# Kernel optimization log

Hardware: AMD Instinct MI355X
Metric: run time of the kernel (lower is better)

The kernel has to match this reference:

```python
import jax, jax.numpy as jnp
import numpy as np

B, S, D = 4, 8192, 768
H, HD = 12, 64
CS, NL = 512, 32


def setup_inputs() -> dict:
    key = jax.random.key(0)
    ks = jax.random.split(key, 9)
    sc = 0.02
    return {
        "x": jax.random.normal(ks[0], (B, S, D), jnp.float32),
        "q_w": jax.random.normal(ks[1], (D, D), jnp.float32) * sc,
        "q_b": jax.random.normal(ks[2], (D,), jnp.float32) * sc,
        "k_w": jax.random.normal(ks[3], (D, D), jnp.float32) * sc,
        "k_b": jax.random.normal(ks[4], (D,), jnp.float32) * sc,
        "v_w": jax.random.normal(ks[5], (D, D), jnp.float32) * sc,
        "v_b": jax.random.normal(ks[6], (D,), jnp.float32) * sc,
        "o_w": jax.random.normal(ks[7], (D, D), jnp.float32) * sc,
        "o_b": jax.random.normal(ks[8], (D,), jnp.float32) * sc,
    }


def reference(x, q_w, q_b, k_w, k_b, v_w, v_b, o_w, o_b):
    # x: (B, S, D); S divisible by CS and NL -> no padding / trimming needed.
    scale = HD ** -0.5
    n_chunks = S // CS
    seg = S // NL
    # Global landmarks: mean-pool NL evenly spaced segments. (B, NL, D)
    landmarks = x.reshape(B, NL, seg, D).mean(axis=2)
    # Q only over local tokens (torch Linear: x @ W^T + b)
    q = (x @ q_w.T + q_b).reshape(B, n_chunks, CS, H, HD)
    x_chunks = x.reshape(B, n_chunks, CS, D)
    # Prepend landmarks to every chunk's KV context: ctx = NL + CS
    lm = jnp.broadcast_to(landmarks[:, None], (B, n_chunks, NL, D))
    kv_ctx = jnp.concatenate([lm, x_chunks], axis=2)  # (B, n_chunks, ctx, D)
    ctx = NL + CS
    k = (kv_ctx @ k_w.T + k_b).reshape(B, n_chunks, ctx, H, HD)
    v = (kv_ctx @ v_w.T + v_b).reshape(B, n_chunks, ctx, H, HD)
    scores = jnp.einsum("bnqhd,bnkhd->bnhqk", q, k) * scale
    attn = jax.nn.softmax(scores, axis=-1)  # dropout=0 (eval)
    out = jnp.einsum("bnhqk,bnkhd->bnqhd", attn, v).reshape(B, S, D)
    return out @ o_w.T + o_b
```

## Files before the change

kernel.cpp:

```cpp
#include <hip/hip_runtime.h>


typedef unsigned short u16;
typedef __attribute__((ext_vector_type(8))) short short8;
typedef __attribute__((ext_vector_type(4))) float f32x4;

__device__ __forceinline__ u16 f2bf(float f) {
    unsigned u = __float_as_uint(f);
    u += 0x7fffu + ((u >> 16) & 1u);
    return (u16)(u >> 16);
}

#define MFMA_BF16(A, B, C) __builtin_amdgcn_mfma_f32_16x16x32_bf16((A), (B), (C), 0, 0, 0)

__device__ __forceinline__ void gload16(const u16* g, const short* l) {
    __builtin_amdgcn_global_load_lds(
        (__attribute__((address_space(1))) void*)g,
        (__attribute__((address_space(3))) void*)l, 16, 0, 0);
}

__global__ __launch_bounds__(256) void k_cvtx(const float* __restrict__ x,
                                              u16* __restrict__ xa,
                                              float* __restrict__ part) {
    const int g = blockIdx.x;
    const int t = threadIdx.x;
    const float* base = x + (size_t)g * 64 * 768;
    u16* ob = xa + (size_t)g * 64 * 768;
    float s0 = 0.f, s1 = 0.f, s2 = 0.f;
    for (int r = 0; r < 64; ++r) {
        const size_t off = (size_t)r * 768;
        const float v0 = base[off + t], v1 = base[off + t + 256], v2 = base[off + t + 512];
        s0 += v0; s1 += v1; s2 += v2;
        ob[off + t] = f2bf(v0); ob[off + t + 256] = f2bf(v1); ob[off + t + 512] = f2bf(v2);
    }
    float* p = part + (size_t)g * 768;
    p[t] = s0; p[t + 256] = s1; p[t + 512] = s2;
}

__global__ void k_lmred(const float* __restrict__ part, u16* __restrict__ xa_lm) {
    const int bl = blockIdx.x;
    const int t = threadIdx.x;
    const float* p = part + (size_t)bl * 4 * 768;
    const float inv = 1.f / 256.f;
    for (int c = t; c < 768; c += 256) {
        const float s = p[c] + p[768 + c] + p[1536 + c] + p[2304 + c];
        xa_lm[(size_t)bl * 768 + c] = f2bf(s * inv);
    }
}

__global__ void k_cvtw(const float* __restrict__ qw, const float* __restrict__ kw,
                       const float* __restrict__ vw, const float* __restrict__ ow,
                       const float* __restrict__ qb, const float* __restrict__ kb,
                       const float* __restrict__ vb,
                       u16* __restrict__ wcat, u16* __restrict__ owb,
                       float* __restrict__ bcat) {
    const int yy = blockIdx.y;
    const int i = blockIdx.x * 256 + threadIdx.x;
    if (yy == 4) {
        if (i < 768)       bcat[i] = qb[i];
        else if (i < 1536) bcat[i] = kb[i - 768];
        else if (i < 2304) bcat[i] = vb[i - 1536];
        return;
    }
    const float* src = (yy == 0) ? qw : (yy == 1) ? kw : (yy == 2) ? vw : ow;
    u16* dst = (yy == 3) ? owb : wcat + (size_t)yy * 589824;
    const float4 v = ((const float4*)src)[i];
    ushort4 o;
    o.x = f2bf(v.x); o.y = f2bf(v.y); o.z = f2bf(v.z); o.w = f2bf(v.w);
    ((ushort4*)dst)[i] = o;
}

template <int MODE>
__global__ __launch_bounds__(512, 1) void k_gemm(
    const u16* __restrict__ A, const u16* __restrict__ Bw, const float* __restrict__ bias,
    u16* __restrict__ qx, u16* __restrict__ ktok, u16* __restrict__ vt,
    u16* __restrict__ klm, u16* __restrict__ vlmt, float* __restrict__ outf)
{
    __shared__ short lA[2 * 16384];
    __shared__ short lB[2 * 16384];
    const int t = threadIdx.x;
    const int wid = t >> 6, lane = t & 63, lr = lane & 15, lg = lane >> 4;
    const int wm = wid >> 2, wn = wid & 3;

    const int gx = gridDim.x;
    const int nwg = gx * gridDim.y;
    const int orig = blockIdx.x + gx * blockIdx.y;
    const int qq = nwg >> 3, rr = nwg & 7, xcd = orig & 7, ii = orig >> 3;
    const int wg = (xcd < rr ? xcd * (qq + 1) : rr * (qq + 1) + (xcd - rr) * qq) + ii;
    const int m0 = (wg / gx) * 256, n0 = (wg % gx) * 256;

    const int MMAX = (MODE == 0) ? 32895 : 32767;
    const int u0 = t, u1 = 512 + t;
    const int r0 = u0 >> 3, c0 = ((u0 & 7) ^ (r0 & 7)) * 8;
    const int r1 = u1 >> 3, c1 = ((u1 & 7) ^ (r1 & 7)) * 8;
    const u16* pA[2][2]; const u16* pB[2][2];
#pragma unroll
    for (int h = 0; h < 2; ++h) {
        int ra0 = m0 + h * 128 + r0; if (ra0 > MMAX) ra0 = MMAX;
        int ra1 = m0 + h * 128 + r1; if (ra1 > MMAX) ra1 = MMAX;
        pA[h][0] = A + (size_t)ra0 * 768 + c0;
        pA[h][1] = A + (size_t)ra1 * 768 + c1;
        pB[h][0] = Bw + (size_t)(n0 + h * 128 + r0) * 768 + c0;
        pB[h][1] = Bw + (size_t)(n0 + h * 128 + r1) * 768 + c1;
    }
    const int sa0 = ((lg) ^ (lr & 7)) * 8;
    const int sa1 = ((4 + lg) ^ (lr & 7)) * 8;

#define STG_A(S, H, T) { gload16(pA[H][0] + (T) * 64, &lA[(S)*16384 + (H)*8192 + wid*512]);      \
                         gload16(pA[H][1] + (T) * 64, &lA[(S)*16384 + (H)*8192 + 4096 + wid*512]); }
#define STG_B(S, H, T) { gload16(pB[H][0] + (T) * 64, &lB[(S)*16384 + (H)*8192 + wid*512]);      \
                         gload16(pB[H][1] + (T) * 64, &lB[(S)*16384 + (H)*8192 + 4096 + wid*512]); }

    f32x4 acc[8][4] = {};
    short8 aq[4][2], bq[4][2];

    STG_A(0, 0, 0); STG_A(0, 1, 0); STG_B(0, 0, 0); STG_B(0, 1, 0);
    STG_A(1, 0, 1); STG_A(1, 1, 1);

#pragma unroll
    for (int T = 0; T < 12; ++T) {
        const int s = T & 1;
        const short* sa = &lA[s * 16384];
        const short* sbm = &lB[s * 16384];
        if (T + 1 < 12) STG_B(s ^ 1, 0, T + 1);
        if (T < 11) asm volatile("s_waitcnt vmcnt(6)" ::: "memory");
        else        asm volatile("s_waitcnt vmcnt(0)" ::: "memory");
        __builtin_amdgcn_s_barrier();
        __builtin_amdgcn_sched_barrier(0);
#pragma unroll
        for (int mf = 0; mf < 4; ++mf) {
            const int rb = (wm * 128 + mf * 16 + lr) * 64;
            aq[mf][0] = *(const short8*)&sa[rb + sa0];
            aq[mf][1] = *(const short8*)&sa[rb + sa1];
        }
#pragma unroll
        for (int nf = 0; nf < 4; ++nf) {
            const int rb = (wn * 64 + nf * 16 + lr) * 64;
            bq[nf][0] = *(const short8*)&sbm[rb + sa0];
            bq[nf][1] = *(const short8*)&sbm[rb + sa1];
        }
        __builtin_amdgcn_s_setprio(1);
#pragma unroll
        for (int mf = 0; mf < 4; ++mf)
#pragma unroll
            for (int nf = 0; nf < 2; ++nf)
#pragma unroll
                for (int kf = 0; kf < 2; ++kf)
                    acc[mf][nf] = MFMA_BF16(aq[mf][kf], bq[nf][kf], acc[mf][nf]);
        __builtin_amdgcn_s_setprio(0);
        if (T + 1 < 12) STG_B(s ^ 1, 1, T + 1);
        __builtin_amdgcn_s_barrier();
        __builtin_amdgcn_s_setprio(1);
#pragma unroll
        for (int mf = 0; mf < 4; ++mf)
#pragma unroll
            for (int nf = 2; nf < 4; ++nf)
#pragma unroll
                for (int kf = 0; kf < 2; ++kf)
                    acc[mf][nf] = MFMA_BF16(aq[mf][kf], bq[nf][kf], acc[mf][nf]);
        __builtin_amdgcn_s_setprio(0);
        __builtin_amdgcn_s_barrier();
#pragma unroll
        for (int mf = 0; mf < 4; ++mf) {
            const int rb = (wm * 128 + (mf + 4) * 16 + lr) * 64;
            aq[mf][0] = *(const short8*)&sa[rb + sa0];
            aq[mf][1] = *(const short8*)&sa[rb + sa1];
        }
        __builtin_amdgcn_s_setprio(1);
#pragma unroll
        for (int mf = 0; mf < 4; ++mf)
#pragma unroll
            for (int nf = 0; nf < 2; ++nf)
#pragma unroll
                for (int kf = 0; kf < 2; ++kf)
                    acc[mf + 4][nf] = MFMA_BF16(aq[mf][kf], bq[nf][kf], acc[mf + 4][nf]);
        __builtin_amdgcn_s_setprio(0);
        __builtin_amdgcn_s_barrier();
        if (T + 2 < 12) { STG_A(s, 0, T + 2); STG_A(s, 1, T + 2); }
        __builtin_amdgcn_s_setprio(1);
#pragma unroll
        for (int mf = 0; mf < 4; ++mf)
#pragma unroll
            for (int nf = 2; nf < 4; ++nf)
#pragma unroll
                for (int kf = 0; kf < 2; ++kf)
                    acc[mf + 4][nf] = MFMA_BF16(aq[mf][kf], bq[nf][kf], acc[mf + 4][nf]);
        __builtin_amdgcn_s_setprio(0);
    }
#undef STG_A
#undef STG_B

    if (MODE == 0) {
        const int region = n0 / 768;
        if (region == 2) {
#pragma unroll
            for (int nf = 0; nf < 4; ++nf) {
                const int gn = n0 + wn * 64 + nf * 16 + lr;
                const float bv = bias[gn];
                const int nn = gn - 1536;
                const int h = nn >> 6, d = nn & 63;
#pragma unroll
                for (int mf = 0; mf < 8; ++mf) {
                    const int gmb = m0 + wm * 128 + mf * 16 + lg * 4;
                    ushort4 w;
                    w.x = f2bf(acc[mf][nf][0] + bv);
                    w.y = f2bf(acc[mf][nf][1] + bv);
                    w.z = f2bf(acc[mf][nf][2] + bv);
                    w.w = f2bf(acc[mf][nf][3] + bv);
                    if (gmb < 32768) {
                        const int b = gmb >> 13, ss = gmb & 8191;
                        *(ushort4*)(vt + ((size_t)(b * 12 + h) * 64 + d) * 8192 + ss) = w;
                    } else if (gmb < 32896) {
                        const int ii2 = gmb - 32768;
                        const int bb = ii2 >> 5, lmr = ii2 & 31;
                        *(ushort4*)(vlmt + ((size_t)(bb * 12 + h) * 64 + d) * 32 + lmr) = w;
                    }
                }
            }
        } else {
            u16* dst = (region == 0) ? qx : ktok;
#pragma unroll
            for (int nf = 0; nf < 4; ++nf) {
                const int gn = n0 + wn * 64 + nf * 16 + lr;
                const int nn = gn - region * 768;
                const int h = nn >> 6, d = nn & 63;
                const float bv = bias[gn];
#pragma unroll
                for (int mf = 0; mf < 8; ++mf) {
                    const int gmb = m0 + wm * 128 + mf * 16 + lg * 4;
#pragma unroll
                    for (int r = 0; r < 4; ++r) {
                        const int gm = gmb + r;
                        const u16 val = f2bf(acc[mf][nf][r] + bv);
                        if (gm < 32768) {
                            const int b = gm >> 13, ss = gm & 8191;
                            dst[((size_t)(b * 12 + h) * 8192 + ss) * 64 + d] = val;
                        } else if (gm < 32896 && region == 1) {
                            const int ii2 = gm - 32768;
                            klm[((size_t)((ii2 >> 5) * 12 + h) * 32 + (ii2 & 31)) * 64 + d] = val;
                        }
                    }
                }
            }
        }
    } else {
#pragma unroll
        for (int nf = 0; nf < 4; ++nf) {
            const int gn = n0 + wn * 64 + nf * 16 + lr;
            const float bvv = bias[gn];
#pragma unroll
            for (int mf = 0; mf < 8; ++mf) {
                const int gmb = m0 + wm * 128 + mf * 16 + lg * 4;
#pragma unroll
                for (int r = 0; r < 4; ++r)
                    outf[(size_t)(gmb + r) * 768 + gn] = acc[mf][nf][r] + bvv;
            }
        }
    }
}

__global__ __launch_bounds__(256) void k_attn(
    const u16* __restrict__ q, const u16* __restrict__ ktok,
    const u16* __restrict__ klm, const u16* __restrict__ vt,
    const u16* __restrict__ vlmt, u16* __restrict__ ao)
{
    __shared__ short kls[2][32 * 72];
    __shared__ short vls[2][64 * 40];
    __shared__ short pls[4][64 * 40];
    const int t = threadIdx.x, wid = t >> 6, l = t & 63, lr = l & 15, lg = l >> 4;
    const int idx = blockIdx.x;
    const int qt = idx & 1;
    const int h  = (idx >> 1) % 12;
    const int cb = (idx >> 1) / 12;
    const int c  = cb & 15, b = cb >> 4;
    const int bh = b * 12 + h;
    const int sb = c * 512 + qt * 256 + wid * 64;

    short8 qf[4][2];
#pragma unroll
    for (int mf = 0; mf < 4; ++mf)
#pragma unroll
        for (int kf = 0; kf < 2; ++kf)
            qf[mf][kf] = *(const short8*)(q + ((size_t)bh * 8192 + sb + mf * 16 + lr) * 64
                                            + kf * 32 + lg * 8);

    f32x4 O[4][4] = {};
    float lsum[4][4] = {};

    short* pw = &pls[wid][0];
    const int kn = t >> 3, kko = (t & 7) * 8;
    const int kctx = (kn < 16) ? (kn * 2) : ((kn - 16) * 2 + 1);
    const int vd = t >> 2, vco = (t & 3) * 8;

    auto kaddr = [&](int ti) -> const u16* {
        if (ti == 0) return klm + ((size_t)bh * 32 + kctx) * 64 + kko;
        return ktok + ((size_t)bh * 8192 + c * 512 + (ti - 1) * 32 + kctx) * 64 + kko;
    };
    auto vaddr = [&](int ti) -> const u16* {
        if (ti == 0) return vlmt + ((size_t)bh * 64 + vd) * 32 + vco;
        return vt + ((size_t)bh * 64 + vd) * 8192 + c * 512 + (ti - 1) * 32 + vco;
    };

    {
        const uint4 rk0 = *(const uint4*)kaddr(0);
        const uint4 rv0 = *(const uint4*)vaddr(0);
        *(uint4*)&kls[0][kn * 72 + kko] = rk0;
        *(uint4*)&vls[0][vd * 40 + vco] = rv0;
    }
    __syncthreads();

    for (int ti = 0; ti < 17; ++ti) {
        const int cur = ti & 1, nxt = cur ^ 1;
        uint4 rk, rv;
        if (ti < 16) { rk = *(const uint4*)kaddr(ti + 1); rv = *(const uint4*)vaddr(ti + 1); }

        f32x4 sc[4][2] = {};
#pragma unroll
        for (int kf = 0; kf < 2; ++kf) {
            const short8 b0 = *(const short8*)&kls[cur][(lr)      * 72 + kf * 32 + lg * 8];
            const short8 b1 = *(const short8*)&kls[cur][(16 + lr) * 72 + kf * 32 + lg * 8];
#pragma unroll
            for (int mf = 0; mf < 4; ++mf) {
                sc[mf][0] = MFMA_BF16(qf[mf][kf], b0, sc[mf][0]);
                sc[mf][1] = MFMA_BF16(qf[mf][kf], b1, sc[mf][1]);
            }
        }

#pragma unroll
        for (int mf = 0; mf < 4; ++mf) {
#pragma unroll
            for (int r = 0; r < 4; ++r) {
                const float p0 = __expf(sc[mf][0][r] * 0.125f);
                const float p1 = __expf(sc[mf][1][r] * 0.125f);
                lsum[mf][r] += p0 + p1;
                unsigned pk;
                asm("v_cvt_pk_bf16_f32 %0, %1, %2" : "=v"(pk) : "v"(p0), "v"(p1));
                const int prow = mf * 16 + lg * 4 + r;
                ((unsigned*)pw)[prow * 20 + lr] = pk;
            }
        }

        short8 vb[4];
#pragma unroll
        for (int df = 0; df < 4; ++df)
            vb[df] = *(const short8*)&vls[cur][(df * 16 + lr) * 40 + lg * 8];
#pragma unroll
        for (int mf = 0; mf < 4; ++mf) {
            const short8 pa = *(const short8*)&pw[(mf * 16 + lr) * 40 + lg * 8];
#pragma unroll
            for (int df = 0; df < 4; ++df)
                O[mf][df] = MFMA_BF16(pa, vb[df], O[mf][df]);
        }

        if (ti < 16) {
            *(uint4*)&kls[nxt][kn * 72 + kko] = rk;
            *(uint4*)&vls[nxt][vd * 40 + vco] = rv;
        }
        __syncthreads();
    }

#pragma unroll
    for (int mf = 0; mf < 4; ++mf)
#pragma unroll
        for (int r = 0; r < 4; ++r) {
            float lv = lsum[mf][r];
            lv += __shfl_xor(lv, 1); lv += __shfl_xor(lv, 2);
            lv += __shfl_xor(lv, 4); lv += __shfl_xor(lv, 8);
            const float inv = 1.f / lv;
            const int srow = sb + mf * 16 + lg * 4 + r;
#pragma unroll
            for (int df = 0; df < 4; ++df)
                ao[((size_t)b * 8192 + srow) * 768 + h * 64 + df * 16 + lr] =
                    f2bf(O[mf][df][r] * inv);
        }
}

extern "C" void kernel_launch(void* const* d_in, const int* in_sizes, int n_in,
                              void* d_out, int out_size, void* d_ws, size_t ws_size,
                              hipStream_t stream)
{
    const float* x  = (const float*)d_in[0];
    const float* qw = (const float*)d_in[1];
    const float* qb = (const float*)d_in[2];
    const float* kw = (const float*)d_in[3];
    const float* kb = (const float*)d_in[4];
    const float* vw = (const float*)d_in[5];
    const float* vb = (const float*)d_in[6];
    const float* ow = (const float*)d_in[7];
    const float* ob = (const float*)d_in[8];
    float* out = (float*)d_out;

    u16* xa     = (u16*)d_ws;
    u16* wcat   = xa + (size_t)32896 * 768;
    u16* owb    = wcat + (size_t)2304 * 768;
    float* bcat = (float*)(owb + (size_t)768 * 768);
    u16* qx     = (u16*)(bcat + 2304);
    u16* ktok   = qx   + (size_t)32768 * 768;
    u16* vt     = ktok + (size_t)32768 * 768;
    u16* klm    = vt + (size_t)32768 * 768;
    u16* vlmt   = klm + 98304;
    float* part = (float*)(vlmt + 98304);
    u16* ao     = xa;

    k_cvtx<<<512, 256, 0, stream>>>(x, xa, part);
    k_lmred<<<128, 256, 0, stream>>>(part, xa + (size_t)32768 * 768);
    k_cvtw<<<dim3(576, 5), 256, 0, stream>>>(qw, kw, vw, ow, qb, kb, vb, wcat, owb, bcat);

    k_gemm<0><<<dim3(9, 129), 512, 0, stream>>>(xa, wcat, bcat,
                                                qx, ktok, vt, klm, vlmt, nullptr);
    k_attn<<<1536, 256, 0, stream>>>(qx, ktok, klm, vt, vlmt, ao);
    k_gemm<1><<<dim3(3, 128), 512, 0, stream>>>(ao, owb, ob,
                                                nullptr, nullptr, nullptr, nullptr, nullptr, out);
}
```

Before: 351.5 us.

## Shrink GEMM tiles to 128x128 with 256 threads and simpler double buffering

The projection GEMMs move from 256x256 tiles on 512-thread blocks to 128x128 tiles on 256-thread blocks with two blocks per CU. The interleaved split-phase pipeline with partial vmcnt waits is replaced by a plain double buffer that waits for all loads, then issues the next stage's loads before computing. The grids grow to match, and the row clamp for the 32896-row input is dropped because the tiles now divide it exactly. This trades per-tile data reuse and finely staged load/compute overlap for more blocks, better occupancy and less tail padding.

```diff
diff --git a/kernel.cpp b/kernel.cpp
--- a/kernel.cpp
+++ b/kernel.cpp
@@ -71,124 +71,79 @@
 }
 
 template <int MODE>
-__global__ __launch_bounds__(512, 1) void k_gemm(
+__global__ __launch_bounds__(256, 2) void k_gemm(
     const u16* __restrict__ A, const u16* __restrict__ Bw, const float* __restrict__ bias,
     u16* __restrict__ qx, u16* __restrict__ ktok, u16* __restrict__ vt,
     u16* __restrict__ klm, u16* __restrict__ vlmt, float* __restrict__ outf)
 {
-    __shared__ short lA[2 * 16384];
-    __shared__ short lB[2 * 16384];
+    __shared__ short lA[2][8192];
+    __shared__ short lB[2][8192];
     const int t = threadIdx.x;
     const int wid = t >> 6, lane = t & 63, lr = lane & 15, lg = lane >> 4;
-    const int wm = wid >> 2, wn = wid & 3;
+    const int wm = wid >> 1, wn = wid & 1;
 
     const int gx = gridDim.x;
     const int nwg = gx * gridDim.y;
     const int orig = blockIdx.x + gx * blockIdx.y;
     const int qq = nwg >> 3, rr = nwg & 7, xcd = orig & 7, ii = orig >> 3;
     const int wg = (xcd < rr ? xcd * (qq + 1) : rr * (qq + 1) + (xcd - rr) * qq) + ii;
-    const int m0 = (wg / gx) * 256, n0 = (wg % gx) * 256;
-
-    const int MMAX = (MODE == 0) ? 32895 : 32767;
-    const int u0 = t, u1 = 512 + t;
-    const int r0 = u0 >> 3, c0 = ((u0 & 7) ^ (r0 & 7)) * 8;
-    const int r1 = u1 >> 3, c1 = ((u1 & 7) ^ (r1 & 7)) * 8;
-    const u16* pA[2][2]; const u16* pB[2][2];
-#pragma unroll
-    for (int h = 0; h < 2; ++h) {
-        int ra0 = m0 + h * 128 + r0; if (ra0 > MMAX) ra0 = MMAX;
-        int ra1 = m0 + h * 128 + r1; if (ra1 > MMAX) ra1 = MMAX;
-        pA[h][0] = A + (size_t)ra0 * 768 + c0;
-        pA[h][1] = A + (size_t)ra1 * 768 + c1;
-        pB[h][0] = Bw + (size_t)(n0 + h * 128 + r0) * 768 + c0;
-        pB[h][1] = Bw + (size_t)(n0 + h * 128 + r1) * 768 + c1;
-    }
-    const int sa0 = ((lg) ^ (lr & 7)) * 8;
+    const int m0 = (wg / gx) * 128, n0 = (wg % gx) * 128;
+
+    const u16* pa[4]; const u16* pb[4];
+#pragma unroll
+    for (int j = 0; j < 4; ++j) {
+        const int u = j * 256 + t;
+        const int row = u >> 3, col = ((u & 7) ^ (row & 7)) * 8;
+        pa[j] = A  + (size_t)(m0 + row) * 768 + col;
+        pb[j] = Bw + (size_t)(n0 + row) * 768 + col;
+    }
+    const int sa0 = (lg ^ (lr & 7)) * 8;
     const int sa1 = ((4 + lg) ^ (lr & 7)) * 8;
 
-#define STG_A(S, H, T) { gload16(pA[H][0] + (T) * 64, &lA[(S)*16384 + (H)*8192 + wid*512]);      \
-                         gload16(pA[H][1] + (T) * 64, &lA[(S)*16384 + (H)*8192 + 4096 + wid*512]); }
-#define STG_B(S, H, T) { gload16(pB[H][0] + (T) * 64, &lB[(S)*16384 + (H)*8192 + wid*512]);      \
-                         gload16(pB[H][1] + (T) * 64, &lB[(S)*16384 + (H)*8192 + 4096 + wid*512]); }
-
-    f32x4 acc[8][4] = {};
-    short8 aq[4][2], bq[4][2];
-
-    STG_A(0, 0, 0); STG_A(0, 1, 0); STG_B(0, 0, 0); STG_B(0, 1, 0);
-    STG_A(1, 0, 1); STG_A(1, 1, 1);
+#define STG(S, T) {                                                       \
+    gload16(pa[0] + (T) * 64, &lA[S][0 * 2048 + wid * 512]);              \
+    gload16(pb[0] + (T) * 64, &lB[S][0 * 2048 + wid * 512]);              \
+    gload16(pa[1] + (T) * 64, &lA[S][1 * 2048 + wid * 512]);              \
+    gload16(pb[1] + (T) * 64, &lB[S][1 * 2048 + wid * 512]);              \
+    gload16(pa[2] + (T) * 64, &lA[S][2 * 2048 + wid * 512]);              \
+    gload16(pb[2] + (T) * 64, &lB[S][2 * 2048 + wid * 512]);              \
+    gload16(pa[3] + (T) * 64, &lA[S][3 * 2048 + wid * 512]);              \
+    gload16(pb[3] + (T) * 64, &lB[S][3 * 2048 + wid * 512]); }
+
+    f32x4 acc[4][4] = {};
+    STG(0, 0);
 
 #pragma unroll
     for (int T = 0; T < 12; ++T) {
         const int s = T & 1;
-        const short* sa = &lA[s * 16384];
-        const short* sbm = &lB[s * 16384];
-        if (T + 1 < 12) STG_B(s ^ 1, 0, T + 1);
-        if (T < 11) asm volatile("s_waitcnt vmcnt(6)" ::: "memory");
-        else        asm volatile("s_waitcnt vmcnt(0)" ::: "memory");
+        asm volatile("s_waitcnt vmcnt(0)" ::: "memory");
         __builtin_amdgcn_s_barrier();
         __builtin_amdgcn_sched_barrier(0);
+        if (T + 1 < 12) STG(s ^ 1, T + 1);
+        short8 aq[4][2], bq[4][2];
 #pragma unroll
         for (int mf = 0; mf < 4; ++mf) {
-            const int rb = (wm * 128 + mf * 16 + lr) * 64;
-            aq[mf][0] = *(const short8*)&sa[rb + sa0];
-            aq[mf][1] = *(const short8*)&sa[rb + sa1];
+            const int rb = (wm * 64 + mf * 16 + lr) * 64;
+            aq[mf][0] = *(const short8*)&lA[s][rb + sa0];
+            aq[mf][1] = *(const short8*)&lA[s][rb + sa1];
         }
 #pragma unroll
         for (int nf = 0; nf < 4; ++nf) {
             const int rb = (wn * 64 + nf * 16 + lr) * 64;
-            bq[nf][0] = *(const short8*)&sbm[rb + sa0];
-            bq[nf][1] = *(const short8*)&sbm[rb + sa1];
+            bq[nf][0] = *(const short8*)&lB[s][rb + sa0];
+            bq[nf][1] = *(const short8*)&lB[s][rb + sa1];
         }
         __builtin_amdgcn_s_setprio(1);
 #pragma unroll
         for (int mf = 0; mf < 4; ++mf)
 #pragma unroll
-            for (int nf = 0; nf < 2; ++nf)
+            for (int nf = 0; nf < 4; ++nf)
 #pragma unroll
                 for (int kf = 0; kf < 2; ++kf)
                     acc[mf][nf] = MFMA_BF16(aq[mf][kf], bq[nf][kf], acc[mf][nf]);
         __builtin_amdgcn_s_setprio(0);
-        if (T + 1 < 12) STG_B(s ^ 1, 1, T + 1);
-        __builtin_amdgcn_s_barrier();
-        __builtin_amdgcn_s_setprio(1);
-#pragma unroll
-        for (int mf = 0; mf < 4; ++mf)
-#pragma unroll
-            for (int nf = 2; nf < 4; ++nf)
-#pragma unroll
-                for (int kf = 0; kf < 2; ++kf)
-                    acc[mf][nf] = MFMA_BF16(aq[mf][kf], bq[nf][kf], acc[mf][nf]);
-        __builtin_amdgcn_s_setprio(0);
-        __builtin_amdgcn_s_barrier();
-#pragma unroll
-        for (int mf = 0; mf < 4; ++mf) {
-            const int rb = (wm * 128 + (mf + 4) * 16 + lr) * 64;
-            aq[mf][0] = *(const short8*)&sa[rb + sa0];
-            aq[mf][1] = *(const short8*)&sa[rb + sa1];
-        }
-        __builtin_amdgcn_s_setprio(1);
-#pragma unroll
-        for (int mf = 0; mf < 4; ++mf)
-#pragma unroll
-            for (int nf = 0; nf < 2; ++nf)
-#pragma unroll
-                for (int kf = 0; kf < 2; ++kf)
-                    acc[mf + 4][nf] = MFMA_BF16(aq[mf][kf], bq[nf][kf], acc[mf + 4][nf]);
-        __builtin_amdgcn_s_setprio(0);
-        __builtin_amdgcn_s_barrier();
-        if (T + 2 < 12) { STG_A(s, 0, T + 2); STG_A(s, 1, T + 2); }
-        __builtin_amdgcn_s_setprio(1);
-#pragma unroll
-        for (int mf = 0; mf < 4; ++mf)
-#pragma unroll
-            for (int nf = 2; nf < 4; ++nf)
-#pragma unroll
-                for (int kf = 0; kf < 2; ++kf)
-                    acc[mf + 4][nf] = MFMA_BF16(aq[mf][kf], bq[nf][kf], acc[mf + 4][nf]);
-        __builtin_amdgcn_s_setprio(0);
-    }
-#undef STG_A
-#undef STG_B
+    }
+#undef STG
 
     if (MODE == 0) {
         const int region = n0 / 768;
@@ -200,8 +155,8 @@
                 const int nn = gn - 1536;
                 const int h = nn >> 6, d = nn & 63;
 #pragma unroll
-                for (int mf = 0; mf < 8; ++mf) {
-                    const int gmb = m0 + wm * 128 + mf * 16 + lg * 4;
+                for (int mf = 0; mf < 4; ++mf) {
+                    const int gmb = m0 + wm * 64 + mf * 16 + lg * 4;
                     ushort4 w;
                     w.x = f2bf(acc[mf][nf][0] + bv);
                     w.y = f2bf(acc[mf][nf][1] + bv);
@@ -210,7 +165,7 @@
                     if (gmb < 32768) {
                         const int b = gmb >> 13, ss = gmb & 8191;
                         *(ushort4*)(vt + ((size_t)(b * 12 + h) * 64 + d) * 8192 + ss) = w;
-                    } else if (gmb < 32896) {
+                    } else {
                         const int ii2 = gmb - 32768;
                         const int bb = ii2 >> 5, lmr = ii2 & 31;
                         *(ushort4*)(vlmt + ((size_t)(bb * 12 + h) * 64 + d) * 32 + lmr) = w;
@@ -226,8 +181,8 @@
                 const int h = nn >> 6, d = nn & 63;
                 const float bv = bias[gn];
 #pragma unroll
-                for (int mf = 0; mf < 8; ++mf) {
-                    const int gmb = m0 + wm * 128 + mf * 16 + lg * 4;
+                for (int mf = 0; mf < 4; ++mf) {
+                    const int gmb = m0 + wm * 64 + mf * 16 + lg * 4;
 #pragma unroll
                     for (int r = 0; r < 4; ++r) {
                         const int gm = gmb + r;
@@ -235,7 +190,7 @@
                         if (gm < 32768) {
                             const int b = gm >> 13, ss = gm & 8191;
                             dst[((size_t)(b * 12 + h) * 8192 + ss) * 64 + d] = val;
-                        } else if (gm < 32896 && region == 1) {
+                        } else if (region == 1) {
                             const int ii2 = gm - 32768;
                             klm[((size_t)((ii2 >> 5) * 12 + h) * 32 + (ii2 & 31)) * 64 + d] = val;
                         }
@@ -249,8 +204,8 @@
             const int gn = n0 + wn * 64 + nf * 16 + lr;
             const float bvv = bias[gn];
 #pragma unroll
-            for (int mf = 0; mf < 8; ++mf) {
-                const int gmb = m0 + wm * 128 + mf * 16 + lg * 4;
+            for (int mf = 0; mf < 4; ++mf) {
+                const int gmb = m0 + wm * 64 + mf * 16 + lg * 4;
 #pragma unroll
                 for (int r = 0; r < 4; ++r)
                     outf[(size_t)(gmb + r) * 768 + gn] = acc[mf][nf][r] + bvv;
@@ -346,10 +301,10 @@
             vb[df] = *(const short8*)&vls[cur][(df * 16 + lr) * 40 + lg * 8];
 #pragma unroll
         for (int mf = 0; mf < 4; ++mf) {
-            const short8 pa = *(const short8*)&pw[(mf * 16 + lr) * 40 + lg * 8];
+            const short8 pa2 = *(const short8*)&pw[(mf * 16 + lr) * 40 + lg * 8];
 #pragma unroll
             for (int df = 0; df < 4; ++df)
-                O[mf][df] = MFMA_BF16(pa, vb[df], O[mf][df]);
+                O[mf][df] = MFMA_BF16(pa2, vb[df], O[mf][df]);
         }
 
         if (ti < 16) {
@@ -406,9 +361,9 @@
     k_lmred<<<128, 256, 0, stream>>>(part, xa + (size_t)32768 * 768);
     k_cvtw<<<dim3(576, 5), 256, 0, stream>>>(qw, kw, vw, ow, qb, kb, vb, wcat, owb, bcat);
 
-    k_gemm<0><<<dim3(9, 129), 512, 0, stream>>>(xa, wcat, bcat,
-                                                qx, ktok, vt, klm, vlmt, nullptr);
+    k_gemm<0><<<dim3(18, 257), 256, 0, stream>>>(xa, wcat, bcat,
+                                                 qx, ktok, vt, klm, vlmt, nullptr);
     k_attn<<<1536, 256, 0, stream>>>(qx, ktok, klm, vt, vlmt, ao);
-    k_gemm<1><<<dim3(3, 128), 512, 0, stream>>>(ao, owb, ob,
+    k_gemm<1><<<dim3(6, 256), 256, 0, stream>>>(ao, owb, ob,
                                                 nullptr, nullptr, nullptr, nullptr, nullptr, out);
 }
```

Result: slower. 382.5 us (+8.8%).
